# Kernel optimization log

Measured on AMD Instinct MI355X. Metric: run time of the kernel, lower is better.

The kernel has to match this reference:

```python
import jax, jax.numpy as jnp
import numpy as np

N = 500000   # nodes per batched graph
D = 64       # per-graph node feature dim (encoded_dims // 2)
P = 1000000  # number of interface candidate pairs
ED = 2 * D   # encoded_dims = 128


def setup_inputs() -> dict:
    key = jax.random.key(0)
    k1, k2, k3, k4, k5, k6 = jax.random.split(key, 6)
    graph1_x = jax.random.normal(k1, (N, D), dtype=jnp.float32)
    graph2_x = jax.random.normal(k2, (N, D), dtype=jnp.float32)
    idx_left = jax.random.randint(k3, (P,), 0, N, dtype=jnp.int32).astype(jnp.int64)
    idx_right = jax.random.randint(k4, (P,), 0, N, dtype=jnp.int32).astype(jnp.int64)
    W1 = jax.random.normal(k5, (ED, ED), dtype=jnp.float32) * (1.0 / np.sqrt(ED))
    b1 = jnp.zeros((ED,), dtype=jnp.float32)
    W2 = jax.random.normal(k6, (1, ED), dtype=jnp.float32) * (1.0 / np.sqrt(ED))
    b2 = jnp.zeros((1,), dtype=jnp.float32)
    return {"graph1_x": graph1_x, "graph2_x": graph2_x,
            "idx_left": idx_left, "idx_right": idx_right,
            "W1": W1, "b1": b1, "W2": W2, "b2": b2}


def reference(graph1_x, graph2_x, idx_left, idx_right, W1, b1, W2, b2):
    # Gather interface node features from both encoded graphs.
    left = graph1_x[idx_left]    # [P, D]
    right = graph2_x[idx_right]  # [P, D]
    x = jnp.concatenate([left, right], axis=1)  # [P, 2D]
    # top_net: Linear -> ReLU -> Dropout(eval: identity) -> Linear
    h = jax.nn.relu(x @ W1.T + b1)  # [P, ED]
    out = h @ W2.T + b2             # [P, 1]
    return out
```

## Files before the change

kernel.cpp:

```cpp
#include <hip/hip_runtime.h>
#include <hip/hip_bf16.h>


typedef __bf16 bf16x8 __attribute__((ext_vector_type(8)));
typedef float f32x16 __attribute__((ext_vector_type(16)));

__device__ __forceinline__ unsigned f2bf(float f) {
  union { float f; unsigned u; } v;
  v.f = f;
  unsigned u = v.u;
  return (u + 0x7fffu + ((u >> 16) & 1u)) >> 16;
}

__global__ __launch_bounds__(256) void w1_frag_kernel(
    const float* __restrict__ W1, uint4* __restrict__ w1f) {
  int t = blockIdx.x * 256 + threadIdx.x;
  int lane = t & 63;
  int nt = (t >> 6) & 3;
  int ks = t >> 8;
  int n = lane & 31, h = lane >> 5;
  const float4* src =
      (const float4*)(W1 + ((nt * 32 + n) * 128 + ks * 16 + h * 8));
  float4 a = src[0], b = src[1];
  uint4 o;
  o.x = f2bf(a.x) | (f2bf(a.y) << 16);
  o.y = f2bf(a.z) | (f2bf(a.w) << 16);
  o.z = f2bf(b.x) | (f2bf(b.y) << 16);
  o.w = f2bf(b.z) | (f2bf(b.w) << 16);
  w1f[t] = o;
}

__global__ __launch_bounds__(256) void cvt_bf16_kernel(
    const float* __restrict__ src, unsigned short* __restrict__ dst, int n8) {
  int i = blockIdx.x * 256 + threadIdx.x;
  const int stride = gridDim.x * 256;
  for (; i < n8; i += stride) {
    const float4* s = (const float4*)(src + (size_t)i * 8);
    float4 a = s[0], b = s[1];
    uint4 o;
    o.x = f2bf(a.x) | (f2bf(a.y) << 16);
    o.y = f2bf(a.z) | (f2bf(a.w) << 16);
    o.z = f2bf(b.x) | (f2bf(b.y) << 16);
    o.w = f2bf(b.z) | (f2bf(b.w) << 16);
    *(uint4*)(dst + (size_t)i * 8) = o;
  }
}

#define LDS_STRIDE 136

template <bool BF16G>
__global__ __launch_bounds__(256, 4) void pip_main_kernel(
    const float* __restrict__ g1, const float* __restrict__ g2,
    const unsigned short* __restrict__ g1b,
    const unsigned short* __restrict__ g2b,
    const int* __restrict__ il, const int* __restrict__ ir,
    const bf16x8* __restrict__ w1f,
    const float* __restrict__ b1, const float* __restrict__ w2,
    const float* __restrict__ b2,
    float* __restrict__ out, int P) {
  __shared__ unsigned short A[128 * LDS_STRIDE];

  const int t = threadIdx.x;
  const int lane = t & 63;
  const int w = t >> 6;
  const int pair0 = blockIdx.x * 128;

  if (BF16G) {
    const int sub = lane & 7;
    const int g = lane >> 3;
    const int side = g & 1;
    const int pairB = (w * 8 + g) >> 1;
    const unsigned short* feat = side ? g2b : g1b;
    const int* idxarr = side ? ir : il;

    int idxv[8];
#pragma unroll
    for (int j = 0; j < 8; ++j) {
      int gp = pair0 + j * 16 + pairB;
      int pidx = (gp < P) ? gp : (P - 1);
      idxv[j] = idxarr[pidx];
    }
#pragma unroll
    for (int j = 0; j < 8; ++j) {
      int pair = j * 16 + pairB;
      uint4 v = *(const uint4*)(feat + (size_t)idxv[j] * 64 + sub * 8);
      *(uint4*)(A + pair * LDS_STRIDE + side * 64 + sub * 8) = v;
    }
  } else {
    const int sub = lane & 15;
    const int g = lane >> 4;
    const int side = g & 1;
    const int pairB = (w * 4 + g) >> 1;
    const float* feat = side ? g2 : g1;
    const int* idxarr = side ? ir : il;

    int idxv[16];
#pragma unroll
    for (int j = 0; j < 16; ++j) {
      int gp = pair0 + j * 8 + pairB;
      int pidx = (gp < P) ? gp : (P - 1);
      idxv[j] = idxarr[pidx];
    }
#pragma unroll
    for (int j = 0; j < 16; ++j) {
      int pair = j * 8 + pairB;
      float4 v = *(const float4*)(feat + (size_t)idxv[j] * 64 + sub * 4);
      unsigned lo = f2bf(v.x) | (f2bf(v.y) << 16);
      unsigned hi = f2bf(v.z) | (f2bf(v.w) << 16);
      *(uint2*)(A + pair * LDS_STRIDE + side * 64 + sub * 4) =
          make_uint2(lo, hi);
    }
  }
  __syncthreads();

  const int n = lane & 31;
  const int h = lane >> 5;

  f32x16 acc[4];
#pragma unroll
  for (int nt = 0; nt < 4; ++nt)
#pragma unroll
    for (int i = 0; i < 16; ++i) acc[nt][i] = 0.0f;

  const unsigned short* Arow = A + (w * 32 + n) * LDS_STRIDE + h * 8;
#pragma unroll
  for (int ks = 0; ks < 8; ++ks) {
    bf16x8 af = *(const bf16x8*)(Arow + ks * 16);
#pragma unroll
    for (int nt = 0; nt < 4; ++nt) {
      bf16x8 bfr = w1f[(ks * 4 + nt) * 64 + lane];
      acc[nt] = __builtin_amdgcn_mfma_f32_32x32x16_bf16(af, bfr, acc[nt], 0, 0, 0);
    }
  }

  float b1v[4], w2v[4];
#pragma unroll
  for (int nt = 0; nt < 4; ++nt) {
    b1v[nt] = b1[nt * 32 + n];
    w2v[nt] = w2[nt * 32 + n];
  }
  const float bias2 = b2[0];

#pragma unroll
  for (int r = 0; r < 16; ++r) {
    float s = 0.0f;
#pragma unroll
    for (int nt = 0; nt < 4; ++nt) {
      float v = acc[nt][r] + b1v[nt];
      v = fmaxf(v, 0.0f);
      s = fmaf(v, w2v[nt], s);
    }
    s += __shfl_xor(s, 1);
    s += __shfl_xor(s, 2);
    s += __shfl_xor(s, 4);
    s += __shfl_xor(s, 8);
    s += __shfl_xor(s, 16);
    if (n == 0) {
      int row = (r & 3) + 8 * (r >> 2) + 4 * h;
      int gp = pair0 + w * 32 + row;
      if (gp < P) out[gp] = s + bias2;
    }
  }
}

extern "C" void kernel_launch(void* const* d_in, const int* in_sizes, int n_in,
                              void* d_out, int out_size, void* d_ws, size_t ws_size,
                              hipStream_t stream) {
  const float* g1 = (const float*)d_in[0];
  const float* g2 = (const float*)d_in[1];
  const int* il = (const int*)d_in[2];
  const int* ir = (const int*)d_in[3];
  const float* W1 = (const float*)d_in[4];
  const float* b1 = (const float*)d_in[5];
  const float* w2 = (const float*)d_in[6];
  const float* b2 = (const float*)d_in[7];
  float* out = (float*)d_out;
  const int P = out_size;

  const int N1 = in_sizes[0] / 64;
  const int N2 = in_sizes[1] / 64;

  const size_t frag_bytes = 32 * 1024;
  const size_t g1b_bytes = (size_t)N1 * 64 * 2;
  const size_t g2b_bytes = (size_t)N2 * 64 * 2;
  const bool bf16path =
      N1 > 0 && N2 > 0 && ws_size >= frag_bytes + g1b_bytes + g2b_bytes;

  w1_frag_kernel<<<8, 256, 0, stream>>>(W1, (uint4*)d_ws);

  const int nblocks = (P + 127) / 128;
  if (bf16path) {
    unsigned short* g1b = (unsigned short*)((char*)d_ws + frag_bytes);
    unsigned short* g2b = g1b + (size_t)N1 * 64;
    cvt_bf16_kernel<<<2048, 256, 0, stream>>>(g1, g1b, N1 * 8);
    cvt_bf16_kernel<<<2048, 256, 0, stream>>>(g2, g2b, N2 * 8);
    pip_main_kernel<true><<<nblocks, 256, 0, stream>>>(
        g1, g2, g1b, g2b, il, ir, (const bf16x8*)d_ws, b1, w2, b2, out, P);
  } else {
    pip_main_kernel<false><<<nblocks, 256, 0, stream>>>(
        g1, g2, nullptr, nullptr, il, ir, (const bf16x8*)d_ws, b1, w2, b2,
        out, P);
  }
}
```

Before: 387.0 us.

## Fuse prep kernels, swizzle LDS tile, and raise main-kernel occupancy

Merges the W1 fragment packing and both fp32-to-bf16 feature conversions into one prep kernel with a non-grid-stride launch and nontemporal loads. This removes two kernel launches and keeps the one-pass streaming input from displacing cache. The LDS tile switches from a padded stride to an XOR-swizzled 256-byte row layout, which is meant to avoid bank conflicts without padding. It also raises the launch bound to 5 blocks per CU, which risks register pressure or spilling.

```diff
diff --git a/kernel.cpp b/kernel.cpp
--- a/kernel.cpp
+++ b/kernel.cpp
@@ -4,6 +4,7 @@
 
 typedef __bf16 bf16x8 __attribute__((ext_vector_type(8)));
 typedef float f32x16 __attribute__((ext_vector_type(16)));
+typedef unsigned u32x4 __attribute__((ext_vector_type(4)));
 
 __device__ __forceinline__ unsigned f2bf(float f) {
   union { float f; unsigned u; } v;
@@ -11,45 +12,62 @@
   unsigned u = v.u;
   return (u + 0x7fffu + ((u >> 16) & 1u)) >> 16;
 }
-
-__global__ __launch_bounds__(256) void w1_frag_kernel(
-    const float* __restrict__ W1, uint4* __restrict__ w1f) {
-  int t = blockIdx.x * 256 + threadIdx.x;
-  int lane = t & 63;
-  int nt = (t >> 6) & 3;
-  int ks = t >> 8;
-  int n = lane & 31, h = lane >> 5;
-  const float4* src =
-      (const float4*)(W1 + ((nt * 32 + n) * 128 + ks * 16 + h * 8));
-  float4 a = src[0], b = src[1];
-  uint4 o;
-  o.x = f2bf(a.x) | (f2bf(a.y) << 16);
-  o.y = f2bf(a.z) | (f2bf(a.w) << 16);
-  o.z = f2bf(b.x) | (f2bf(b.y) << 16);
-  o.w = f2bf(b.z) | (f2bf(b.w) << 16);
-  w1f[t] = o;
-}
-
-__global__ __launch_bounds__(256) void cvt_bf16_kernel(
-    const float* __restrict__ src, unsigned short* __restrict__ dst, int n8) {
-  int i = blockIdx.x * 256 + threadIdx.x;
-  const int stride = gridDim.x * 256;
-  for (; i < n8; i += stride) {
-    const float4* s = (const float4*)(src + (size_t)i * 8);
-    float4 a = s[0], b = s[1];
+__device__ __forceinline__ unsigned u2bf(unsigned u) {
+  return (u + 0x7fffu + ((u >> 16) & 1u)) >> 16;
+}
+__device__ __forceinline__ unsigned pack2(unsigned lo, unsigned hi) {
+  return u2bf(lo) | (u2bf(hi) << 16);
+}
+
+__global__ __launch_bounds__(256) void prep_kernel(
+    const float* __restrict__ g1, const float* __restrict__ g2,
+    const float* __restrict__ W1,
+    unsigned short* __restrict__ g1b, unsigned short* __restrict__ g2b,
+    uint4* __restrict__ w1f, int n8_1, int n8_2) {
+  const int t = blockIdx.x * 256 + threadIdx.x;
+
+  if (t < 2048) {
+    int lane = t & 63;
+    int nt = (t >> 6) & 3;
+    int ks = t >> 8;
+    int n = lane & 31, h = lane >> 5;
+    const float4* src =
+        (const float4*)(W1 + ((nt * 32 + n) * 128 + ks * 16 + h * 8));
+    float4 a = src[0], b = src[1];
     uint4 o;
     o.x = f2bf(a.x) | (f2bf(a.y) << 16);
     o.y = f2bf(a.z) | (f2bf(a.w) << 16);
     o.z = f2bf(b.x) | (f2bf(b.y) << 16);
     o.w = f2bf(b.z) | (f2bf(b.w) << 16);
-    *(uint4*)(dst + (size_t)i * 8) = o;
-  }
-}
-
-#define LDS_STRIDE 136
+    w1f[t] = o;
+  }
+
+  const int total = n8_1 + n8_2;
+  const int c0 = t * 2;
+#pragma unroll
+  for (int u = 0; u < 2; ++u) {
+    int c = c0 + u;
+    if (c < total) {
+      const float* src;
+      unsigned short* dst;
+      int lc;
+      if (c < n8_1) { src = g1; dst = g1b; lc = c; }
+      else          { src = g2; dst = g2b; lc = c - n8_1; }
+      const u32x4* sp = (const u32x4*)(src + (size_t)lc * 8);
+      u32x4 a = __builtin_nontemporal_load(sp);
+      u32x4 b = __builtin_nontemporal_load(sp + 1);
+      u32x4 o;
+      o.x = pack2(a.x, a.y);
+      o.y = pack2(a.z, a.w);
+      o.z = pack2(b.x, b.y);
+      o.w = pack2(b.z, b.w);
+      *(u32x4*)(dst + (size_t)lc * 8) = o;
+    }
+  }
+}
 
 template <bool BF16G>
-__global__ __launch_bounds__(256, 4) void pip_main_kernel(
+__global__ __launch_bounds__(256, 5) void pip_main_kernel(
     const float* __restrict__ g1, const float* __restrict__ g2,
     const unsigned short* __restrict__ g1b,
     const unsigned short* __restrict__ g2b,
@@ -58,7 +76,7 @@
     const float* __restrict__ b1, const float* __restrict__ w2,
     const float* __restrict__ b2,
     float* __restrict__ out, int P) {
-  __shared__ unsigned short A[128 * LDS_STRIDE];
+  __shared__ unsigned char A[128 * 256];
 
   const int t = threadIdx.x;
   const int lane = t & 63;
@@ -84,7 +102,8 @@
     for (int j = 0; j < 8; ++j) {
       int pair = j * 16 + pairB;
       uint4 v = *(const uint4*)(feat + (size_t)idxv[j] * 64 + sub * 8);
-      *(uint4*)(A + pair * LDS_STRIDE + side * 64 + sub * 8) = v;
+      int g16 = side * 8 + sub;
+      *(uint4*)(&A[pair * 256 + ((g16 ^ (pair & 7)) << 4)]) = v;
     }
   } else {
     const int sub = lane & 15;
@@ -107,7 +126,8 @@
       float4 v = *(const float4*)(feat + (size_t)idxv[j] * 64 + sub * 4);
       unsigned lo = f2bf(v.x) | (f2bf(v.y) << 16);
       unsigned hi = f2bf(v.z) | (f2bf(v.w) << 16);
-      *(uint2*)(A + pair * LDS_STRIDE + side * 64 + sub * 4) =
+      int g16 = side * 8 + (sub >> 1);
+      *(uint2*)(&A[pair * 256 + ((g16 ^ (pair & 7)) << 4) + ((sub & 1) << 3)]) =
           make_uint2(lo, hi);
     }
   }
@@ -122,10 +142,11 @@
 #pragma unroll
     for (int i = 0; i < 16; ++i) acc[nt][i] = 0.0f;
 
-  const unsigned short* Arow = A + (w * 32 + n) * LDS_STRIDE + h * 8;
+  const unsigned char* Abase = &A[(w * 32 + n) * 256];
+  const int rk = n & 7;
 #pragma unroll
   for (int ks = 0; ks < 8; ++ks) {
-    bf16x8 af = *(const bf16x8*)(Arow + ks * 16);
+    bf16x8 af = *(const bf16x8*)(Abase + (((ks * 2 + h) ^ rk) << 4));
 #pragma unroll
     for (int nt = 0; nt < 4; ++nt) {
       bf16x8 bfr = w1f[(ks * 4 + nt) * 64 + lane];
@@ -186,14 +207,19 @@
   const bool bf16path =
       N1 > 0 && N2 > 0 && ws_size >= frag_bytes + g1b_bytes + g2b_bytes;
 
-  w1_frag_kernel<<<8, 256, 0, stream>>>(W1, (uint4*)d_ws);
+  unsigned short* g1b = (unsigned short*)((char*)d_ws + frag_bytes);
+  unsigned short* g2b = g1b + (size_t)N1 * 64;
+
+  const int n8_1 = bf16path ? N1 * 8 : 0;
+  const int n8_2 = bf16path ? N2 * 8 : 0;
+  const int total = n8_1 + n8_2;
+  int prep_blocks = ((total + 1) / 2 + 255) / 256;
+  if (prep_blocks < 8) prep_blocks = 8;
+  prep_kernel<<<prep_blocks, 256, 0, stream>>>(g1, g2, W1, g1b, g2b,
+                                               (uint4*)d_ws, n8_1, n8_2);
 
   const int nblocks = (P + 127) / 128;
   if (bf16path) {
-    unsigned short* g1b = (unsigned short*)((char*)d_ws + frag_bytes);
-    unsigned short* g2b = g1b + (size_t)N1 * 64;
-    cvt_bf16_kernel<<<2048, 256, 0, stream>>>(g1, g1b, N1 * 8);
-    cvt_bf16_kernel<<<2048, 256, 0, stream>>>(g2, g2b, N2 * 8);
     pip_main_kernel<true><<<nblocks, 256, 0, stream>>>(
         g1, g2, g1b, g2b, il, ir, (const bf16x8*)d_ws, b1, w2, b2, out, P);
   } else {
```

After: 408.0 us. 1.05x slower.

## Drop bf16 pre-conversion passes; gather fp32 directly into per-wave swizzled LDS

Applied to the files above, without the earlier changes.

Removes the two full-graph fp32-to-bf16 conversion kernels and gathers fp32 rows directly, converting in registers. Each wave now stages only its own 32 pairs in a private XOR-swizzled LDS tile, so the block-wide barrier becomes a wave-local LDS wait, and launch bounds raise the occupancy target. This trades the streaming conversion traffic for doubled-size random gathers of fp32 rows.

```diff
diff --git a/kernel.cpp b/kernel.cpp
--- a/kernel.cpp
+++ b/kernel.cpp
@@ -1,5 +1,4 @@
 #include <hip/hip_runtime.h>
-#include <hip/hip_bf16.h>
 
 
 typedef __bf16 bf16x8 __attribute__((ext_vector_type(8)));
@@ -30,88 +29,47 @@
   w1f[t] = o;
 }
 
-__global__ __launch_bounds__(256) void cvt_bf16_kernel(
-    const float* __restrict__ src, unsigned short* __restrict__ dst, int n8) {
-  int i = blockIdx.x * 256 + threadIdx.x;
-  const int stride = gridDim.x * 256;
-  for (; i < n8; i += stride) {
-    const float4* s = (const float4*)(src + (size_t)i * 8);
-    float4 a = s[0], b = s[1];
-    uint4 o;
-    o.x = f2bf(a.x) | (f2bf(a.y) << 16);
-    o.y = f2bf(a.z) | (f2bf(a.w) << 16);
-    o.z = f2bf(b.x) | (f2bf(b.y) << 16);
-    o.w = f2bf(b.z) | (f2bf(b.w) << 16);
-    *(uint4*)(dst + (size_t)i * 8) = o;
-  }
-}
-
-#define LDS_STRIDE 136
-
-template <bool BF16G>
-__global__ __launch_bounds__(256, 4) void pip_main_kernel(
+__global__ __launch_bounds__(256, 5) void pip_main_kernel(
     const float* __restrict__ g1, const float* __restrict__ g2,
-    const unsigned short* __restrict__ g1b,
-    const unsigned short* __restrict__ g2b,
     const int* __restrict__ il, const int* __restrict__ ir,
     const bf16x8* __restrict__ w1f,
     const float* __restrict__ b1, const float* __restrict__ w2,
     const float* __restrict__ b2,
     float* __restrict__ out, int P) {
-  __shared__ unsigned short A[128 * LDS_STRIDE];
+  __shared__ unsigned char A[4][8192];
 
   const int t = threadIdx.x;
   const int lane = t & 63;
   const int w = t >> 6;
   const int pair0 = blockIdx.x * 128;
 
-  if (BF16G) {
-    const int sub = lane & 7;
-    const int g = lane >> 3;
-    const int side = g & 1;
-    const int pairB = (w * 8 + g) >> 1;
-    const unsigned short* feat = side ? g2b : g1b;
-    const int* idxarr = side ? ir : il;
+  const int sub = lane & 15;
+  const int g = lane >> 4;
+  const int side = g & 1;
+  const int phalf = g >> 1;
+  const float* feat = side ? g2 : g1;
+  const int* idxarr = side ? ir : il;
 
-    int idxv[8];
+  int idxv[16];
 #pragma unroll
-    for (int j = 0; j < 8; ++j) {
-      int gp = pair0 + j * 16 + pairB;
-      int pidx = (gp < P) ? gp : (P - 1);
-      idxv[j] = idxarr[pidx];
-    }
+  for (int j = 0; j < 16; ++j) {
+    int gp = pair0 + w * 32 + j * 2 + phalf;
+    int pidx = (gp < P) ? gp : (P - 1);
+    idxv[j] = idxarr[pidx];
+  }
+
+  unsigned char* Aw = &A[w][0];
 #pragma unroll
-    for (int j = 0; j < 8; ++j) {
-      int pair = j * 16 + pairB;
-      uint4 v = *(const uint4*)(feat + (size_t)idxv[j] * 64 + sub * 8);
-      *(uint4*)(A + pair * LDS_STRIDE + side * 64 + sub * 8) = v;
-    }
-  } else {
-    const int sub = lane & 15;
-    const int g = lane >> 4;
-    const int side = g & 1;
-    const int pairB = (w * 4 + g) >> 1;
-    const float* feat = side ? g2 : g1;
-    const int* idxarr = side ? ir : il;
-
-    int idxv[16];
-#pragma unroll
-    for (int j = 0; j < 16; ++j) {
-      int gp = pair0 + j * 8 + pairB;
-      int pidx = (gp < P) ? gp : (P - 1);
-      idxv[j] = idxarr[pidx];
-    }
-#pragma unroll
-    for (int j = 0; j < 16; ++j) {
-      int pair = j * 8 + pairB;
-      float4 v = *(const float4*)(feat + (size_t)idxv[j] * 64 + sub * 4);
-      unsigned lo = f2bf(v.x) | (f2bf(v.y) << 16);
-      unsigned hi = f2bf(v.z) | (f2bf(v.w) << 16);
-      *(uint2*)(A + pair * LDS_STRIDE + side * 64 + sub * 4) =
-          make_uint2(lo, hi);
-    }
+  for (int j = 0; j < 16; ++j) {
+    int pl = j * 2 + phalf;
+    float4 v = *(const float4*)(feat + (size_t)idxv[j] * 64 + sub * 4);
+    unsigned lo = f2bf(v.x) | (f2bf(v.y) << 16);
+    unsigned hi = f2bf(v.z) | (f2bf(v.w) << 16);
+    int g16 = side * 8 + (sub >> 1);
+    *(uint2*)(Aw + pl * 256 + ((g16 ^ (pl & 7)) << 4) + ((sub & 1) << 3)) =
+        make_uint2(lo, hi);
   }
-  __syncthreads();
+  asm volatile("s_waitcnt lgkmcnt(0)" ::: "memory");
 
   const int n = lane & 31;
   const int h = lane >> 5;
@@ -122,10 +80,11 @@
 #pragma unroll
     for (int i = 0; i < 16; ++i) acc[nt][i] = 0.0f;
 
-  const unsigned short* Arow = A + (w * 32 + n) * LDS_STRIDE + h * 8;
+  const unsigned char* Abase = Aw + n * 256;
+  const int rk = n & 7;
 #pragma unroll
   for (int ks = 0; ks < 8; ++ks) {
-    bf16x8 af = *(const bf16x8*)(Arow + ks * 16);
+    bf16x8 af = *(const bf16x8*)(Abase + (((ks * 2 + h) ^ rk) << 4));
 #pragma unroll
     for (int nt = 0; nt < 4; ++nt) {
       bf16x8 bfr = w1f[(ks * 4 + nt) * 64 + lane];
@@ -177,28 +136,9 @@
   float* out = (float*)d_out;
   const int P = out_size;
 
-  const int N1 = in_sizes[0] / 64;
-  const int N2 = in_sizes[1] / 64;
-
-  const size_t frag_bytes = 32 * 1024;
-  const size_t g1b_bytes = (size_t)N1 * 64 * 2;
-  const size_t g2b_bytes = (size_t)N2 * 64 * 2;
-  const bool bf16path =
-      N1 > 0 && N2 > 0 && ws_size >= frag_bytes + g1b_bytes + g2b_bytes;
-
   w1_frag_kernel<<<8, 256, 0, stream>>>(W1, (uint4*)d_ws);
 
   const int nblocks = (P + 127) / 128;
-  if (bf16path) {
-    unsigned short* g1b = (unsigned short*)((char*)d_ws + frag_bytes);
-    unsigned short* g2b = g1b + (size_t)N1 * 64;
-    cvt_bf16_kernel<<<2048, 256, 0, stream>>>(g1, g1b, N1 * 8);
-    cvt_bf16_kernel<<<2048, 256, 0, stream>>>(g2, g2b, N2 * 8);
-    pip_main_kernel<true><<<nblocks, 256, 0, stream>>>(
-        g1, g2, g1b, g2b, il, ir, (const bf16x8*)d_ws, b1, w2, b2, out, P);
-  } else {
-    pip_main_kernel<false><<<nblocks, 256, 0, stream>>>(
-        g1, g2, nullptr, nullptr, il, ir, (const bf16x8*)d_ws, b1, w2, b2,
-        out, P);
-  }
+  pip_main_kernel<<<nblocks, 256, 0, stream>>>(
+      g1, g2, il, ir, (const bf16x8*)d_ws, b1, w2, b2, out, P);
 }
```

Result: faster. 342.4 us (-11.5%).
